# Optimization experiments

Measured on AMD Instinct MI355X. Metric: run time of the kernel, lower is better.

## Reference

```python
import jax, jax.numpy as jnp
import numpy as np

HIDDEN = 2048
HEADS = 32
HEAD_DIM = HIDDEN // HEADS  # 64
MAX_POS = 512
TABLE = 2 * MAX_POS - 1  # 1023


def setup_inputs() -> dict:
    key = jax.random.key(0)
    k = jax.random.split(key, 6)
    B, S = 16, 512
    return {
        "hidden_states": jax.random.normal(k[0], (B, S, HIDDEN), dtype=jnp.float32),
        "wq": jax.random.normal(k[1], (HIDDEN, HIDDEN), dtype=jnp.float32) * 0.02,
        "wk": jax.random.normal(k[2], (HIDDEN, HIDDEN), dtype=jnp.float32) * 0.02,
        "wv": jax.random.normal(k[3], (HIDDEN, HIDDEN), dtype=jnp.float32) * 0.02,
        "wo": jax.random.normal(k[4], (HIDDEN, HIDDEN), dtype=jnp.float32) * 0.02,
        "rel_pos": jax.random.normal(k[5], (TABLE, HEAD_DIM), dtype=jnp.float32),
    }


def _rel_bias(rel_pos, seq_len):
    pos = jnp.arange(seq_len)
    rel = pos[None, :] - pos[:, None] + (MAX_POS - 1)  # [S, S]
    rel = jnp.clip(rel, 0, TABLE - 1)
    return rel_pos[rel].mean(axis=-1)  # [S, S]


def reference(hidden_states, wq, wk, wv, wo, rel_pos):
    B, S, _ = hidden_states.shape
    scale = jnp.sqrt(jnp.float32(HEAD_DIM))
    # nn.Linear(x) = x @ W.T
    q = (hidden_states @ wq.T).reshape(B, S, HEADS, HEAD_DIM).transpose(0, 2, 1, 3)
    k = (hidden_states @ wk.T).reshape(B, S, HEADS, HEAD_DIM).transpose(0, 2, 1, 3)
    v = (hidden_states @ wv.T).reshape(B, S, HEADS, HEAD_DIM).transpose(0, 2, 1, 3)
    scores = jnp.einsum("bhqd,bhkd->bhqk", q, k) / scale
    scores = scores + _rel_bias(rel_pos, S)[None, None]  # seq_len <= 512 path
    attn = jax.nn.softmax(scores, axis=-1)
    ctx = jnp.einsum("bhqk,bhkd->bhqd", attn, v)
    ctx = ctx.transpose(0, 2, 1, 3).reshape(B, S, HIDDEN)
    return ctx @ wo.T
```

## Files before the change

### kernel.cpp

```cpp
#include <hip/hip_runtime.h>

typedef __attribute__((ext_vector_type(8))) short bf16x8;
typedef __attribute__((ext_vector_type(4))) float f32x4;

#define DEVI __device__ __forceinline__

DEVI unsigned short f2bf(float f) {
  union { float f; unsigned u; } v; v.f = f;
  unsigned r = v.u + 0x7FFFu + ((v.u >> 16) & 1u);
  return (unsigned short)(r >> 16);
}

DEVI void gload16(const void* g, void* l) {
  __builtin_amdgcn_global_load_lds(
      (const __attribute__((address_space(1))) unsigned int*)g,
      (__attribute__((address_space(3))) unsigned int*)l, 16, 0, 0);
}

#define MFMA16(a, b, c) __builtin_amdgcn_mfma_f32_16x16x32_bf16(a, b, c, 0, 0, 0)

__global__ void cvt_kernel(const float* __restrict__ in,
                           unsigned short* __restrict__ out, int n4) {
  int i = blockIdx.x * blockDim.x + threadIdx.x;
  if (i < n4) {
    float4 v = ((const float4*)in)[i];
    ushort4 o;
    o.x = f2bf(v.x); o.y = f2bf(v.y); o.z = f2bf(v.z); o.w = f2bf(v.w);
    ((ushort4*)out)[i] = o;
  }
}

__global__ void bias_kernel(const float* __restrict__ rel_pos,
                            float* __restrict__ bias1d) {
  int t = blockIdx.x * blockDim.x + threadIdx.x;
  if (t < 1023) {
    const float* r = rel_pos + t * 64;
    float s = 0.f;
#pragma unroll
    for (int d = 0; d < 64; ++d) s += r[d];
    bias1d[t] = s * (1.44269504f / 64.0f);
  }
}

template <int MODE>
__global__ __launch_bounds__(512, 2) void gemm256(
    const unsigned short* __restrict__ A, const unsigned short* __restrict__ B,
    void* __restrict__ Cout) {
  __shared__ unsigned short As[2][16384];
  __shared__ unsigned short Bs[2][16384];

  const int tid = threadIdx.x;
  const int logical = (blockIdx.x & 7) * 32 + (blockIdx.x >> 3);
  const int nt = logical & 7, mt = logical >> 3;
  const int m0 = mt * 256, n0 = nt * 256;
  const int lane = tid & 63, wid = tid >> 6;
  const int wr = wid >> 2, wc = wid & 3;
  const int g = lane >> 4, c = lane & 15;

  const unsigned short* Ag = A + (size_t)m0 * 2048u;
  const unsigned short* Bg = B + (size_t)n0 * 2048u;

  auto stage_half = [&](int buf, int kt, int h) {
    const int hh = h & 1;
    const unsigned short* gb = (h < 2) ? Ag : Bg;
    unsigned short* lb = (h < 2) ? &As[buf][hh * 8192] : &Bs[buf][hh * 8192];
#pragma unroll
    for (int ch = 0; ch < 2; ++ch) {
      const int slot = ch * 512 + tid;
      const int row = slot >> 3;
      const int j = (slot & 7) ^ (row & 7);
      gload16(gb + (size_t)(hh * 128 + row) * 2048u + kt * 64 + j * 8,
              lb + slot * 8);
    }
  };

  f32x4 acc[8][4];
#pragma unroll
  for (int i = 0; i < 8; ++i)
#pragma unroll
    for (int j = 0; j < 4; ++j) acc[i][j] = (f32x4){0.f, 0.f, 0.f, 0.f};

  stage_half(0, 0, 0); stage_half(0, 0, 1);
  stage_half(0, 0, 2); stage_half(0, 0, 3);
  stage_half(1, 1, 0); stage_half(1, 1, 1);
  asm volatile("s_waitcnt vmcnt(4)" ::: "memory");
  __builtin_amdgcn_sched_barrier(0);
  __builtin_amdgcn_s_barrier();

  bf16x8 af[4][2], bq0[2][2], bq1[2][2];

  for (int kt = 0; kt < 32; ++kt) {
    const int buf = kt & 1;
    const unsigned short* Ab = &As[buf][0];
    const unsigned short* Bb = &Bs[buf][0];

#pragma unroll
    for (int mi = 0; mi < 4; ++mi) {
      const int r = wr * 128 + mi * 16 + c;
#pragma unroll
      for (int kk = 0; kk < 2; ++kk)
        af[mi][kk] = *(const bf16x8*)(Ab + r * 64 + (((kk * 4 + g) ^ (r & 7)) * 8));
    }
#pragma unroll
    for (int ni = 0; ni < 2; ++ni) {
      const int r = wc * 64 + ni * 16 + c;
#pragma unroll
      for (int kk = 0; kk < 2; ++kk)
        bq0[ni][kk] = *(const bf16x8*)(Bb + r * 64 + (((kk * 4 + g) ^ (r & 7)) * 8));
    }
    if (kt + 1 < 32) stage_half(buf ^ 1, kt + 1, 2);
    __builtin_amdgcn_s_barrier();
    __builtin_amdgcn_s_setprio(1);
#pragma unroll
    for (int mi = 0; mi < 4; ++mi)
#pragma unroll
      for (int ni = 0; ni < 2; ++ni)
#pragma unroll
        for (int kk = 0; kk < 2; ++kk)
          acc[mi][ni] = MFMA16(af[mi][kk], bq0[ni][kk], acc[mi][ni]);
    __builtin_amdgcn_s_setprio(0);
    __builtin_amdgcn_s_barrier();

#pragma unroll
    for (int ni = 0; ni < 2; ++ni) {
      const int r = wc * 64 + (ni + 2) * 16 + c;
#pragma unroll
      for (int kk = 0; kk < 2; ++kk)
        bq1[ni][kk] = *(const bf16x8*)(Bb + r * 64 + (((kk * 4 + g) ^ (r & 7)) * 8));
    }
    if (kt + 1 < 32) stage_half(buf ^ 1, kt + 1, 3);
    __builtin_amdgcn_s_barrier();
    __builtin_amdgcn_s_setprio(1);
#pragma unroll
    for (int mi = 0; mi < 4; ++mi)
#pragma unroll
      for (int ni = 0; ni < 2; ++ni)
#pragma unroll
        for (int kk = 0; kk < 2; ++kk)
          acc[mi][ni + 2] = MFMA16(af[mi][kk], bq1[ni][kk], acc[mi][ni + 2]);
    __builtin_amdgcn_s_setprio(0);
    __builtin_amdgcn_s_barrier();

#pragma unroll
    for (int mi = 0; mi < 4; ++mi) {
      const int r = wr * 128 + (mi + 4) * 16 + c;
#pragma unroll
      for (int kk = 0; kk < 2; ++kk)
        af[mi][kk] = *(const bf16x8*)(Ab + r * 64 + (((kk * 4 + g) ^ (r & 7)) * 8));
    }
    __builtin_amdgcn_s_barrier();
    __builtin_amdgcn_s_setprio(1);
#pragma unroll
    for (int mi = 0; mi < 4; ++mi)
#pragma unroll
      for (int ni = 0; ni < 2; ++ni)
#pragma unroll
        for (int kk = 0; kk < 2; ++kk)
          acc[mi + 4][ni] = MFMA16(af[mi][kk], bq0[ni][kk], acc[mi + 4][ni]);
    __builtin_amdgcn_s_setprio(0);
    __builtin_amdgcn_s_barrier();

    if (kt + 2 < 32) { stage_half(buf, kt + 2, 0); stage_half(buf, kt + 2, 1); }
    if (kt < 30) {
      asm volatile("s_waitcnt vmcnt(4)" ::: "memory");
    } else {
      asm volatile("s_waitcnt vmcnt(0)" ::: "memory");
    }
    __builtin_amdgcn_sched_barrier(0);
    __builtin_amdgcn_s_barrier();
    __builtin_amdgcn_s_setprio(1);
#pragma unroll
    for (int mi = 0; mi < 4; ++mi)
#pragma unroll
      for (int ni = 0; ni < 2; ++ni)
#pragma unroll
        for (int kk = 0; kk < 2; ++kk)
          acc[mi + 4][ni + 2] = MFMA16(af[mi][kk], bq1[ni][kk], acc[mi + 4][ni + 2]);
    __builtin_amdgcn_s_setprio(0);
    __builtin_amdgcn_s_barrier();
  }

  const int rbase = m0 + wr * 128 + g * 4;
  const int cbase = n0 + wc * 64 + c;
  if (MODE == 0) {
    float* O = (float*)Cout;
#pragma unroll
    for (int mi = 0; mi < 8; ++mi)
#pragma unroll
      for (int ni = 0; ni < 4; ++ni)
#pragma unroll
        for (int rr = 0; rr < 4; ++rr)
          O[(size_t)(rbase + mi * 16 + rr) * 2048u + (cbase + ni * 16)] =
              acc[mi][ni][rr];
  } else if (MODE == 1) {
    unsigned short* O = (unsigned short*)Cout;
#pragma unroll
    for (int mi = 0; mi < 8; ++mi)
#pragma unroll
      for (int ni = 0; ni < 4; ++ni)
#pragma unroll
        for (int rr = 0; rr < 4; ++rr)
          O[(size_t)(rbase + mi * 16 + rr) * 2048u + (cbase + ni * 16)] =
              f2bf(acc[mi][ni][rr]);
  } else {
    unsigned short* O = (unsigned short*)Cout;
#pragma unroll
    for (int mi = 0; mi < 8; ++mi)
#pragma unroll
      for (int ni = 0; ni < 4; ++ni) {
        const int row = rbase + mi * 16;
        const int col = cbase + ni * 16;
        const int bq_ = row >> 9, s = row & 511;
        const int hh = col >> 6, dd = col & 63;
        ushort4 o;
        o.x = f2bf(acc[mi][ni][0]);
        o.y = f2bf(acc[mi][ni][1]);
        o.z = f2bf(acc[mi][ni][2]);
        o.w = f2bf(acc[mi][ni][3]);
        *(ushort4*)(O + ((size_t)((bq_ * 32 + hh) * 64 + dd) << 9) + s) = o;
      }
  }
}

__global__ __launch_bounds__(256, 3) void attn_kernel(
    const unsigned short* __restrict__ Q, const unsigned short* __restrict__ K,
    const unsigned short* __restrict__ VT, const float* __restrict__ bias1d,
    unsigned short* __restrict__ CTX) {
  __shared__ unsigned short Ksh[2][4096];
  __shared__ unsigned short Vsh[2][4096];
  __shared__ unsigned short Pb[4][2048];
  __shared__ float bl[1024];

  const int tid = threadIdx.x;
  const int wave = tid >> 6;
  const int lane = tid & 63;
  const int g = lane >> 4, c = lane & 15;

  const int logical = (blockIdx.x & 7) * 256 + (blockIdx.x >> 3);
  const int qc = logical & 3;
  const int bh = logical >> 2;
  const int b = bh >> 5, h = bh & 31;
  const int qrow0 = qc * 128 + wave * 32;

  for (int i = tid; i < 1023; i += 256) bl[i] = bias1d[i];

  bf16x8 aq[2][2];
  {
    const unsigned short* qb =
        Q + (size_t)(b * 512 + qrow0 + c) * 2048u + h * 64 + g * 8;
#pragma unroll
    for (int mi = 0; mi < 2; ++mi)
#pragma unroll
      for (int kk = 0; kk < 2; ++kk)
        aq[mi][kk] = *(const bf16x8*)(qb + mi * 16 * 2048 + kk * 32);
  }

  const unsigned short* kgb = K + (size_t)(b * 512) * 2048u + h * 64;
  const unsigned short* vgb = VT + (size_t)(bh * 64) * 512u;

  auto stage = [&](int buf, int kt) {
#pragma unroll
    for (int half = 0; half < 2; ++half) {
      const int slot = half * 256 + wave * 64 + lane;
      const int row = slot >> 3;
      const int j = (slot & 7) ^ (row & 7);
      gload16(kgb + (size_t)(kt * 64 + row) * 2048u + j * 8,
              &Ksh[buf][slot * 8]);
      gload16(vgb + (size_t)row * 512u + kt * 64 + j * 8, &Vsh[buf][slot * 8]);
    }
  };

  f32x4 o[2][4];
#pragma unroll
  for (int mi = 0; mi < 2; ++mi)
#pragma unroll
    for (int di = 0; di < 4; ++di) o[mi][di] = (f32x4){0.f, 0.f, 0.f, 0.f};
  float lreg[2][4];
#pragma unroll
  for (int mi = 0; mi < 2; ++mi)
#pragma unroll
    for (int rr = 0; rr < 4; ++rr) lreg[mi][rr] = 0.f;

  stage(0, 0);
  __syncthreads();

  const float SSCALE = 0.125f * 1.44269504f;

  for (int kt = 0; kt < 8; ++kt) {
    const int buf = kt & 1;
    if (kt < 7) stage(buf ^ 1, kt + 1);

    f32x4 s[2][4];
#pragma unroll
    for (int ni = 0; ni < 4; ++ni) {
      const unsigned short* kr = &Ksh[buf][(ni * 16 + c) * 64];
      bf16x8 bk0 = *(const bf16x8*)(kr + ((0 + g) ^ (c & 7)) * 8);
      bf16x8 bk1 = *(const bf16x8*)(kr + ((4 + g) ^ (c & 7)) * 8);
#pragma unroll
      for (int mi = 0; mi < 2; ++mi) {
        f32x4 z = (f32x4){0.f, 0.f, 0.f, 0.f};
        z = MFMA16(aq[mi][0], bk0, z);
        z = MFMA16(aq[mi][1], bk1, z);
        s[mi][ni] = z;
      }
    }

    unsigned short* pw = &Pb[wave][0];
#pragma unroll
    for (int mi = 0; mi < 2; ++mi)
#pragma unroll
      for (int rr = 0; rr < 4; ++rr) {
        const int prow = mi * 16 + g * 4 + rr;
        const int off0 = kt * 64 + c - (qrow0 + prow) + 511;
        float e0 = __builtin_amdgcn_exp2f(s[mi][0][rr] * SSCALE + bl[off0]);
        float e1 = __builtin_amdgcn_exp2f(s[mi][1][rr] * SSCALE + bl[off0 + 16]);
        float e2 = __builtin_amdgcn_exp2f(s[mi][2][rr] * SSCALE + bl[off0 + 32]);
        float e3 = __builtin_amdgcn_exp2f(s[mi][3][rr] * SSCALE + bl[off0 + 48]);
        lreg[mi][rr] += (e0 + e1) + (e2 + e3);
        const int rx = prow * 64, sw = (c >> 3) ^ (prow & 7), cl = c & 7;
        pw[rx + ((0 ^ sw) * 8 | cl)] = f2bf(e0);
        pw[rx + ((2 ^ sw) * 8 | cl)] = f2bf(e1);
        pw[rx + ((4 ^ sw) * 8 | cl)] = f2bf(e2);
        pw[rx + ((6 ^ sw) * 8 | cl)] = f2bf(e3);
      }

#pragma unroll
    for (int kk = 0; kk < 2; ++kk) {
      bf16x8 pa0 =
          *(const bf16x8*)(pw + (0 + c) * 64 + ((kk * 4 + g) ^ (c & 7)) * 8);
      bf16x8 pa1 =
          *(const bf16x8*)(pw + (16 + c) * 64 + ((kk * 4 + g) ^ (c & 7)) * 8);
#pragma unroll
      for (int di = 0; di < 4; ++di) {
        bf16x8 vb = *(const bf16x8*)(&Vsh[buf][(di * 16 + c) * 64 +
                                               ((kk * 4 + g) ^ (c & 7)) * 8]);
        o[0][di] = MFMA16(pa0, vb, o[0][di]);
        o[1][di] = MFMA16(pa1, vb, o[1][di]);
      }
    }
    __syncthreads();
  }

#pragma unroll
  for (int mi = 0; mi < 2; ++mi)
#pragma unroll
    for (int rr = 0; rr < 4; ++rr) {
      float l = lreg[mi][rr];
      l += __shfl_xor(l, 1);
      l += __shfl_xor(l, 2);
      l += __shfl_xor(l, 4);
      l += __shfl_xor(l, 8);
      const float rl = __builtin_amdgcn_rcpf(l);
      unsigned short* ob =
          CTX + (size_t)(b * 512 + qrow0 + mi * 16 + g * 4 + rr) * 2048u +
          h * 64 + c;
#pragma unroll
      for (int di = 0; di < 4; ++di) ob[di * 16] = f2bf(o[mi][di][rr] * rl);
    }
}

extern "C" void kernel_launch(void* const* d_in, const int* in_sizes, int n_in,
                              void* d_out, int out_size, void* d_ws,
                              size_t ws_size, hipStream_t stream) {
  const float* x = (const float*)d_in[0];
  const float* wq = (const float*)d_in[1];
  const float* wk = (const float*)d_in[2];
  const float* wv = (const float*)d_in[3];
  const float* wo = (const float*)d_in[4];
  const float* rel = (const float*)d_in[5];

  char* ws = (char*)d_ws;
  unsigned short* xb = (unsigned short*)(ws);
  unsigned short* wqb = (unsigned short*)(ws + 33554432);
  unsigned short* wkb = wqb + 4194304;
  unsigned short* wvb = wkb + 4194304;
  unsigned short* wob = wvb + 4194304;
  unsigned short* qb = (unsigned short*)(ws + 67108864);
  unsigned short* kb = qb + 16777216;
  unsigned short* vt = kb + 16777216;
  float* bias1 = (float*)(ws + 167772160);
  unsigned short* ctx = xb;

  cvt_kernel<<<16384, 256, 0, stream>>>(x, xb, 4194304);
  cvt_kernel<<<4096, 256, 0, stream>>>(wq, wqb, 1048576);
  cvt_kernel<<<4096, 256, 0, stream>>>(wk, wkb, 1048576);
  cvt_kernel<<<4096, 256, 0, stream>>>(wv, wvb, 1048576);
  cvt_kernel<<<4096, 256, 0, stream>>>(wo, wob, 1048576);
  bias_kernel<<<4, 256, 0, stream>>>(rel, bias1);

  gemm256<1><<<256, 512, 0, stream>>>(xb, wqb, qb);
  gemm256<1><<<256, 512, 0, stream>>>(xb, wkb, kb);
  gemm256<2><<<256, 512, 0, stream>>>(xb, wvb, vt);

  attn_kernel<<<2048, 256, 0, stream>>>(qb, kb, vt, bias1, ctx);

  gemm256<0><<<256, 512, 0, stream>>>(ctx, wob, (float*)d_out);
}
```

Measured before the change: 359.7 us.

## Fuse QKV projections into one GEMM launch and rework LDS read scheduling

The three Q/K/V projection GEMMs become one launch over a concatenated N=6144 weight space (wq, wk, wv are contiguous in the workspace). The epilogue routes each tile to Q, K or transposed V by column. The GEMM inner loop now uses inline-asm ds_read_b128 with explicit lgkmcnt waits and sched barriers, reorders the MFMA loops to put kk outermost, and splits the next-stage A loads across two phases to spread global traffic. This aims to cut launch tail effects and improve overlap, at the cost of fragile hand-scheduled waits.

```diff
diff --git a/kernel.cpp b/kernel.cpp
--- a/kernel.cpp
+++ b/kernel.cpp
@@ -15,6 +15,14 @@
   __builtin_amdgcn_global_load_lds(
       (const __attribute__((address_space(1))) unsigned int*)g,
       (__attribute__((address_space(3))) unsigned int*)l, 16, 0, 0);
+}
+
+DEVI bf16x8 lread(const unsigned short* p) {
+  bf16x8 r;
+  asm volatile("ds_read_b128 %0, %1"
+               : "=v"(r)
+               : "v"((const __attribute__((address_space(3))) unsigned short*)p));
+  return r;
 }
 
 #define MFMA16(a, b, c) __builtin_amdgcn_mfma_f32_16x16x32_bf16(a, b, c, 0, 0, 0)
@@ -42,16 +50,16 @@
   }
 }
 
-template <int MODE>
+template <int MODE, int NT>
 __global__ __launch_bounds__(512, 2) void gemm256(
     const unsigned short* __restrict__ A, const unsigned short* __restrict__ B,
-    void* __restrict__ Cout) {
+    void* __restrict__ Cout, void* __restrict__ Cout2, void* __restrict__ Cout3) {
   __shared__ unsigned short As[2][16384];
   __shared__ unsigned short Bs[2][16384];
 
   const int tid = threadIdx.x;
-  const int logical = (blockIdx.x & 7) * 32 + (blockIdx.x >> 3);
-  const int nt = logical & 7, mt = logical >> 3;
+  const int logical = (blockIdx.x & 7) * (4 * NT) + (blockIdx.x >> 3);
+  const int nt = logical % NT, mt = logical / NT;
   const int m0 = mt * 256, n0 = nt * 256;
   const int lane = tid & 63, wid = tid >> 6;
   const int wr = wid >> 2, wc = wid & 3;
@@ -99,24 +107,26 @@
       const int r = wr * 128 + mi * 16 + c;
 #pragma unroll
       for (int kk = 0; kk < 2; ++kk)
-        af[mi][kk] = *(const bf16x8*)(Ab + r * 64 + (((kk * 4 + g) ^ (r & 7)) * 8));
+        af[mi][kk] = lread(Ab + r * 64 + (((kk * 4 + g) ^ (r & 7)) * 8));
     }
 #pragma unroll
     for (int ni = 0; ni < 2; ++ni) {
       const int r = wc * 64 + ni * 16 + c;
 #pragma unroll
       for (int kk = 0; kk < 2; ++kk)
-        bq0[ni][kk] = *(const bf16x8*)(Bb + r * 64 + (((kk * 4 + g) ^ (r & 7)) * 8));
+        bq0[ni][kk] = lread(Bb + r * 64 + (((kk * 4 + g) ^ (r & 7)) * 8));
     }
     if (kt + 1 < 32) stage_half(buf ^ 1, kt + 1, 2);
     __builtin_amdgcn_s_barrier();
+    asm volatile("s_waitcnt lgkmcnt(0)");
+    __builtin_amdgcn_sched_barrier(0);
     __builtin_amdgcn_s_setprio(1);
 #pragma unroll
-    for (int mi = 0; mi < 4; ++mi)
-#pragma unroll
-      for (int ni = 0; ni < 2; ++ni)
-#pragma unroll
-        for (int kk = 0; kk < 2; ++kk)
+    for (int kk = 0; kk < 2; ++kk)
+#pragma unroll
+      for (int mi = 0; mi < 4; ++mi)
+#pragma unroll
+        for (int ni = 0; ni < 2; ++ni)
           acc[mi][ni] = MFMA16(af[mi][kk], bq0[ni][kk], acc[mi][ni]);
     __builtin_amdgcn_s_setprio(0);
     __builtin_amdgcn_s_barrier();
@@ -126,17 +136,19 @@
       const int r = wc * 64 + (ni + 2) * 16 + c;
 #pragma unroll
       for (int kk = 0; kk < 2; ++kk)
-        bq1[ni][kk] = *(const bf16x8*)(Bb + r * 64 + (((kk * 4 + g) ^ (r & 7)) * 8));
+        bq1[ni][kk] = lread(Bb + r * 64 + (((kk * 4 + g) ^ (r & 7)) * 8));
     }
     if (kt + 1 < 32) stage_half(buf ^ 1, kt + 1, 3);
     __builtin_amdgcn_s_barrier();
+    asm volatile("s_waitcnt lgkmcnt(0)");
+    __builtin_amdgcn_sched_barrier(0);
     __builtin_amdgcn_s_setprio(1);
 #pragma unroll
-    for (int mi = 0; mi < 4; ++mi)
-#pragma unroll
-      for (int ni = 0; ni < 2; ++ni)
-#pragma unroll
-        for (int kk = 0; kk < 2; ++kk)
+    for (int kk = 0; kk < 2; ++kk)
+#pragma unroll
+      for (int mi = 0; mi < 4; ++mi)
+#pragma unroll
+        for (int ni = 0; ni < 2; ++ni)
           acc[mi][ni + 2] = MFMA16(af[mi][kk], bq1[ni][kk], acc[mi][ni + 2]);
     __builtin_amdgcn_s_setprio(0);
     __builtin_amdgcn_s_barrier();
@@ -146,21 +158,24 @@
       const int r = wr * 128 + (mi + 4) * 16 + c;
 #pragma unroll
       for (int kk = 0; kk < 2; ++kk)
-        af[mi][kk] = *(const bf16x8*)(Ab + r * 64 + (((kk * 4 + g) ^ (r & 7)) * 8));
-    }
-    __builtin_amdgcn_s_barrier();
+        af[mi][kk] = lread(Ab + r * 64 + (((kk * 4 + g) ^ (r & 7)) * 8));
+    }
+    if (kt + 2 < 32) stage_half(buf, kt + 2, 0);
+    __builtin_amdgcn_s_barrier();
+    asm volatile("s_waitcnt lgkmcnt(0)");
+    __builtin_amdgcn_sched_barrier(0);
     __builtin_amdgcn_s_setprio(1);
 #pragma unroll
-    for (int mi = 0; mi < 4; ++mi)
-#pragma unroll
-      for (int ni = 0; ni < 2; ++ni)
-#pragma unroll
-        for (int kk = 0; kk < 2; ++kk)
+    for (int kk = 0; kk < 2; ++kk)
+#pragma unroll
+      for (int mi = 0; mi < 4; ++mi)
+#pragma unroll
+        for (int ni = 0; ni < 2; ++ni)
           acc[mi + 4][ni] = MFMA16(af[mi][kk], bq0[ni][kk], acc[mi + 4][ni]);
     __builtin_amdgcn_s_setprio(0);
     __builtin_amdgcn_s_barrier();
 
-    if (kt + 2 < 32) { stage_half(buf, kt + 2, 0); stage_half(buf, kt + 2, 1); }
+    if (kt + 2 < 32) stage_half(buf, kt + 2, 1);
     if (kt < 30) {
       asm volatile("s_waitcnt vmcnt(4)" ::: "memory");
     } else {
@@ -170,11 +185,11 @@
     __builtin_amdgcn_s_barrier();
     __builtin_amdgcn_s_setprio(1);
 #pragma unroll
-    for (int mi = 0; mi < 4; ++mi)
-#pragma unroll
-      for (int ni = 0; ni < 2; ++ni)
-#pragma unroll
-        for (int kk = 0; kk < 2; ++kk)
+    for (int kk = 0; kk < 2; ++kk)
+#pragma unroll
+      for (int mi = 0; mi < 4; ++mi)
+#pragma unroll
+        for (int ni = 0; ni < 2; ++ni)
           acc[mi + 4][ni + 2] = MFMA16(af[mi][kk], bq1[ni][kk], acc[mi + 4][ni + 2]);
     __builtin_amdgcn_s_setprio(0);
     __builtin_amdgcn_s_barrier();
@@ -192,33 +207,36 @@
         for (int rr = 0; rr < 4; ++rr)
           O[(size_t)(rbase + mi * 16 + rr) * 2048u + (cbase + ni * 16)] =
               acc[mi][ni][rr];
-  } else if (MODE == 1) {
-    unsigned short* O = (unsigned short*)Cout;
-#pragma unroll
-    for (int mi = 0; mi < 8; ++mi)
-#pragma unroll
-      for (int ni = 0; ni < 4; ++ni)
-#pragma unroll
-        for (int rr = 0; rr < 4; ++rr)
-          O[(size_t)(rbase + mi * 16 + rr) * 2048u + (cbase + ni * 16)] =
-              f2bf(acc[mi][ni][rr]);
   } else {
-    unsigned short* O = (unsigned short*)Cout;
-#pragma unroll
-    for (int mi = 0; mi < 8; ++mi)
-#pragma unroll
-      for (int ni = 0; ni < 4; ++ni) {
-        const int row = rbase + mi * 16;
-        const int col = cbase + ni * 16;
-        const int bq_ = row >> 9, s = row & 511;
-        const int hh = col >> 6, dd = col & 63;
-        ushort4 o;
-        o.x = f2bf(acc[mi][ni][0]);
-        o.y = f2bf(acc[mi][ni][1]);
-        o.z = f2bf(acc[mi][ni][2]);
-        o.w = f2bf(acc[mi][ni][3]);
-        *(ushort4*)(O + ((size_t)((bq_ * 32 + hh) * 64 + dd) << 9) + s) = o;
-      }
+    const int qsel = cbase >> 11;
+    if (qsel < 2) {
+      unsigned short* O = (unsigned short*)(qsel == 0 ? Cout : Cout2);
+#pragma unroll
+      for (int mi = 0; mi < 8; ++mi)
+#pragma unroll
+        for (int ni = 0; ni < 4; ++ni)
+#pragma unroll
+          for (int rr = 0; rr < 4; ++rr)
+            O[(size_t)(rbase + mi * 16 + rr) * 2048u +
+              ((cbase + ni * 16) & 2047)] = f2bf(acc[mi][ni][rr]);
+    } else {
+      unsigned short* O = (unsigned short*)Cout3;
+#pragma unroll
+      for (int mi = 0; mi < 8; ++mi)
+#pragma unroll
+        for (int ni = 0; ni < 4; ++ni) {
+          const int row = rbase + mi * 16;
+          const int col = (cbase + ni * 16) & 2047;
+          const int bq_ = row >> 9, s = row & 511;
+          const int hh = col >> 6, dd = col & 63;
+          ushort4 o;
+          o.x = f2bf(acc[mi][ni][0]);
+          o.y = f2bf(acc[mi][ni][1]);
+          o.z = f2bf(acc[mi][ni][2]);
+          o.w = f2bf(acc[mi][ni][3]);
+          *(ushort4*)(O + ((size_t)((bq_ * 32 + hh) * 64 + dd) << 9) + s) = o;
+        }
+    }
   }
 }
 
@@ -388,11 +406,10 @@
   cvt_kernel<<<4096, 256, 0, stream>>>(wo, wob, 1048576);
   bias_kernel<<<4, 256, 0, stream>>>(rel, bias1);
 
-  gemm256<1><<<256, 512, 0, stream>>>(xb, wqb, qb);
-  gemm256<1><<<256, 512, 0, stream>>>(xb, wkb, kb);
-  gemm256<2><<<256, 512, 0, stream>>>(xb, wvb, vt);
+  gemm256<3, 24><<<768, 512, 0, stream>>>(xb, wqb, qb, kb, vt);
 
   attn_kernel<<<2048, 256, 0, stream>>>(qb, kb, vt, bias1, ctx);
 
-  gemm256<0><<<256, 512, 0, stream>>>(ctx, wob, (float*)d_out);
-}
+  gemm256<0, 8><<<256, 512, 0, stream>>>(ctx, wob, (float*)d_out, nullptr,
+                                         nullptr);
+}
```

Result: faster. 348.3 us (-3.2%).
